# Performance work log

Measured on AMD Instinct MI355X. Metric: run time of the kernel, lower is better.

Reference implementation:

```python
import jax, jax.numpy as jnp
import numpy as np

ALPHA = 0.2          # LeakyReLU negative slope
NEG_BIG = -9e15      # mask fill value from the original code
N, IN_F, OUT_F = 8192, 128, 64


def setup_inputs() -> dict:
    key = jax.random.key(0)
    k1, k2, k3, k4 = jax.random.split(key, 4)
    h = jax.random.normal(k1, (N, IN_F), dtype=jnp.float32)
    adj = jax.random.randint(k2, (N, N), 0, 2, dtype=jnp.int32)
    W = jax.random.normal(k3, (IN_F, OUT_F), dtype=jnp.float32) * 0.1
    a = jax.random.normal(k4, (2 * OUT_F, 1), dtype=jnp.float32) * 0.1
    return {"h": h, "adj": adj, "W": W, "a": a}


def reference(h, adj, W, a):
    # Wh: [N, F]
    Wh = h @ W
    # e_ij = leakyrelu([Wh_i ; Wh_j] . a) = leakyrelu(Wh_i.a1 + Wh_j.a2)
    # (identical math to the original NxNx2F concat, without materializing it)
    a1 = a[:OUT_F, 0]   # [F]
    a2 = a[OUT_F:, 0]   # [F]
    s1 = Wh @ a1        # [N]
    s2 = Wh @ a2        # [N]
    e = jax.nn.leaky_relu(s1[:, None] + s2[None, :], negative_slope=ALPHA)  # [N, N]
    e = jnp.where(adj > 0, e, jnp.float32(NEG_BIG))
    attention = jax.nn.softmax(e, axis=1)
    # dropout is identity at inference (training=False)
    h_prime = attention @ Wh  # [N, F]
    return jax.nn.elu(h_prime)  # concat=True -> elu
```

## Files before the change

### kernel.cpp

```cpp
#include <hip/hip_runtime.h>
#include <hip/hip_bf16.h>

#define N 8192
#define IN_F 128
#define OUT_F 64
#define LRELU_ALPHA 0.2f
#define NEG_BIG -9000000000000000.0f

typedef __attribute__((ext_vector_type(8))) short short8;
typedef __attribute__((ext_vector_type(4))) float float4v;

__device__ __forceinline__ unsigned short bf16_bits(float x) {
  unsigned u = __builtin_bit_cast(unsigned, x);
  u += 0x7fffu + ((u >> 16) & 1u);
  return (unsigned short)(u >> 16);
}

__global__ __launch_bounds__(256) void prep_kernel(
    const float* __restrict__ h, const float* __restrict__ W,
    const float* __restrict__ a, float* __restrict__ s1,
    float* __restrict__ s2, unsigned short* __restrict__ whT) {
  const int tid = threadIdx.x;
  const int row = blockIdx.x * 4 + (tid >> 6);
  const int k = tid & 63;
  const float* hr = h + row * IN_F;
  float acc = 0.f;
#pragma unroll 8
  for (int c = 0; c < IN_F; ++c) acc = fmaf(hr[c], W[c * OUT_F + k], acc);
  whT[(long)k * N + row] = bf16_bits(acc);
  float p1 = acc * a[k];
  float p2 = acc * a[OUT_F + k];
#pragma unroll
  for (int off = 32; off > 0; off >>= 1) {
    p1 += __shfl_xor(p1, off);
    p2 += __shfl_xor(p2, off);
  }
  if (k == 0) { s1[row] = p1; s2[row] = p2; }
}

__global__ __launch_bounds__(512) void gat_kernel(
    const int* __restrict__ adj, const float* __restrict__ s1,
    const float* __restrict__ s2, const unsigned short* __restrict__ whT,
    float* __restrict__ out) {
  __shared__ float lds_acc[8][16][65];
  __shared__ float lds_l[8][16];

  const int tid = threadIdx.x;
  const int wave = tid >> 6;
  const int lane = tid & 63;
  const int r16 = lane & 15;
  const int quad = lane >> 4;
  const int row0 = blockIdx.x * 16;
  const int col0 = wave * 1024;

  const float s1r = s1[row0 + r16];
  const long adj_base = (long)(row0 + r16) * N;

  float lsum = 0.f;
  float4v acc0 = {0.f, 0.f, 0.f, 0.f};
  float4v acc1 = {0.f, 0.f, 0.f, 0.f};
  float4v acc2 = {0.f, 0.f, 0.f, 0.f};
  float4v acc3 = {0.f, 0.f, 0.f, 0.f};

  for (int t = 0; t < 32; ++t) {
    const int j0 = col0 + t * 32 + quad * 8;
    const int4* ap = (const int4*)(adj + adj_base + j0);
    const int4 a0 = ap[0];
    const int4 a1 = ap[1];
    const float4* sp = (const float4*)(s2 + j0);
    const float4 s20 = sp[0], s21 = sp[1];
    const unsigned short* bp = whT + (long)r16 * N + j0;
    const short8 b0 = *(const short8*)(bp + 0L * 16 * N);
    const short8 b1 = *(const short8*)(bp + 1L * 16 * N);
    const short8 b2 = *(const short8*)(bp + 2L * 16 * N);
    const short8 b3 = *(const short8*)(bp + 3L * 16 * N);

    float se[8] = {s20.x, s20.y, s20.z, s20.w, s21.x, s21.y, s21.z, s21.w};
    int am[8] = {a0.x, a0.y, a0.z, a0.w, a1.x, a1.y, a1.z, a1.w};
    short8 afrag;
#pragma unroll
    for (int i = 0; i < 8; ++i) {
      float tv = s1r + se[i];
      tv = fmaxf(tv, LRELU_ALPHA * tv);
      const float e = am[i] > 0 ? tv : NEG_BIG;
      const float p = __expf(e);
      lsum += p;
      afrag[i] = (short)bf16_bits(p);
    }
    acc0 = __builtin_amdgcn_mfma_f32_16x16x32_bf16(afrag, b0, acc0, 0, 0, 0);
    acc1 = __builtin_amdgcn_mfma_f32_16x16x32_bf16(afrag, b1, acc1, 0, 0, 0);
    acc2 = __builtin_amdgcn_mfma_f32_16x16x32_bf16(afrag, b2, acc2, 0, 0, 0);
    acc3 = __builtin_amdgcn_mfma_f32_16x16x32_bf16(afrag, b3, acc3, 0, 0, 0);
  }

  lsum += __shfl_xor(lsum, 16);
  lsum += __shfl_xor(lsum, 32);
  if (lane < 16) lds_l[wave][lane] = lsum;
#pragma unroll
  for (int reg = 0; reg < 4; ++reg) {
    const int r = quad * 4 + reg;
    lds_acc[wave][r][0 * 16 + r16] = acc0[reg];
    lds_acc[wave][r][1 * 16 + r16] = acc1[reg];
    lds_acc[wave][r][2 * 16 + r16] = acc2[reg];
    lds_acc[wave][r][3 * 16 + r16] = acc3[reg];
  }
  __syncthreads();

#pragma unroll
  for (int o = tid; o < 16 * 64; o += 512) {
    const int r = o >> 6, k = o & 63;
    float S = 0.f, L = 0.f;
#pragma unroll
    for (int w = 0; w < 8; ++w) {
      S += lds_acc[w][r][k];
      L += lds_l[w][r];
    }
    const float v = S / L;
    out[(long)(row0 + r) * OUT_F + k] = v > 0.f ? v : expm1f(v);
  }
}

extern "C" void kernel_launch(void* const* d_in, const int* in_sizes, int n_in,
                              void* d_out, int out_size, void* d_ws, size_t ws_size,
                              hipStream_t stream) {
  const float* h = (const float*)d_in[0];
  const int* adj = (const int*)d_in[1];
  const float* W = (const float*)d_in[2];
  const float* a = (const float*)d_in[3];
  float* out = (float*)d_out;

  float* s1 = (float*)d_ws;
  float* s2 = s1 + N;
  unsigned short* whT = (unsigned short*)(s2 + N);

  prep_kernel<<<N / 4, 256, 0, stream>>>(h, W, a, s1, s2, whT);
  gat_kernel<<<N / 16, 512, 0, stream>>>(adj, s1, s2, whT, out);
}
```

Measured before the change: 447.8 us.

## Coalesce adjacency loads via LDS staging and pre-swizzle Wh into MFMA fragment order

The GAT kernel now has each lane read contiguous int4 chunks of adjacency across 16 rows, computes exp weights, and stages the bf16 probabilities in a padded LDS buffer, then reads MFMA A-fragments from LDS. A new repack kernel rearranges Wh into fragment-contiguous order so B-fragment loads are fully coalesced. The row-sum is computed with an extra MFMA against a vector of ones instead of shuffles, and masked entries are set to zero directly rather than exp of a large negative. This adds one extra small kernel launch, LDS traffic and register pressure in exchange for better global load coalescing on the dominant adjacency read.

```diff
diff --git a/kernel.cpp b/kernel.cpp
--- a/kernel.cpp
+++ b/kernel.cpp
@@ -5,10 +5,10 @@
 #define IN_F 128
 #define OUT_F 64
 #define LRELU_ALPHA 0.2f
-#define NEG_BIG -9000000000000000.0f
 
 typedef __attribute__((ext_vector_type(8))) short short8;
 typedef __attribute__((ext_vector_type(4))) float float4v;
+typedef __attribute__((ext_vector_type(4))) unsigned short ushortx4;
 
 __device__ __forceinline__ unsigned short bf16_bits(float x) {
   unsigned u = __builtin_bit_cast(unsigned, x);
@@ -38,84 +38,100 @@
   if (k == 0) { s1[row] = p1; s2[row] = p2; }
 }
 
-__global__ __launch_bounds__(512) void gat_kernel(
+__global__ __launch_bounds__(256) void repack_kernel(
+    const unsigned short* __restrict__ whT, unsigned short* __restrict__ whF) {
+  const int f = blockIdx.x * 256 + threadIdx.x;
+  const int lane = f & 63, tt = (f >> 6) & 3, c = f >> 8;
+  const int r16 = lane & 15, quad = lane >> 4;
+  const short8 v = *(const short8*)(whT + (long)(tt * 16 + r16) * N + c * 32 + quad * 8);
+  *(short8*)(whF + (long)f * 8) = v;
+}
+
+#define PSTR 264
+#define WREG (16 * PSTR * 2)
+
+__global__ __launch_bounds__(512, 4) void gat_kernel(
     const int* __restrict__ adj, const float* __restrict__ s1,
-    const float* __restrict__ s2, const unsigned short* __restrict__ whT,
+    const float* __restrict__ s2, const unsigned short* __restrict__ whF,
     float* __restrict__ out) {
-  __shared__ float lds_acc[8][16][65];
-  __shared__ float lds_l[8][16];
+  __shared__ __align__(16) unsigned char lds_raw[8 * WREG];
+  const int tid = threadIdx.x;
+  const int w = tid >> 6, L = tid & 63;
+  const int r16 = L & 15, quad = L >> 4;
+  const int row0 = blockIdx.x * 16;
+  unsigned short* pl = (unsigned short*)(lds_raw + w * WREG);
 
-  const int tid = threadIdx.x;
-  const int wave = tid >> 6;
-  const int lane = tid & 63;
-  const int r16 = lane & 15;
-  const int quad = lane >> 4;
-  const int row0 = blockIdx.x * 16;
-  const int col0 = wave * 1024;
+  float s1r[16];
+#pragma unroll
+  for (int r = 0; r < 16; ++r) s1r[r] = s1[row0 + r];
 
-  const float s1r = s1[row0 + r16];
-  const long adj_base = (long)(row0 + r16) * N;
-
-  float lsum = 0.f;
   float4v acc0 = {0.f, 0.f, 0.f, 0.f};
   float4v acc1 = {0.f, 0.f, 0.f, 0.f};
   float4v acc2 = {0.f, 0.f, 0.f, 0.f};
   float4v acc3 = {0.f, 0.f, 0.f, 0.f};
+  float4v accL = {0.f, 0.f, 0.f, 0.f};
+  const short ONE = (short)0x3F80;
+  const short8 ones = {ONE, ONE, ONE, ONE, ONE, ONE, ONE, ONE};
 
-  for (int t = 0; t < 32; ++t) {
-    const int j0 = col0 + t * 32 + quad * 8;
-    const int4* ap = (const int4*)(adj + adj_base + j0);
-    const int4 a0 = ap[0];
-    const int4 a1 = ap[1];
-    const float4* sp = (const float4*)(s2 + j0);
-    const float4 s20 = sp[0], s21 = sp[1];
-    const unsigned short* bp = whT + (long)r16 * N + j0;
-    const short8 b0 = *(const short8*)(bp + 0L * 16 * N);
-    const short8 b1 = *(const short8*)(bp + 1L * 16 * N);
-    const short8 b2 = *(const short8*)(bp + 2L * 16 * N);
-    const short8 b3 = *(const short8*)(bp + 3L * 16 * N);
-
-    float se[8] = {s20.x, s20.y, s20.z, s20.w, s21.x, s21.y, s21.z, s21.w};
-    int am[8] = {a0.x, a0.y, a0.z, a0.w, a1.x, a1.y, a1.z, a1.w};
-    short8 afrag;
+  for (int s = 0; s < 4; ++s) {
+    const int col = w * 1024 + s * 256 + L * 4;
+    const float4 s2v = *(const float4*)(s2 + col);
+    int4 av[16];
 #pragma unroll
-    for (int i = 0; i < 8; ++i) {
-      float tv = s1r + se[i];
-      tv = fmaxf(tv, LRELU_ALPHA * tv);
-      const float e = am[i] > 0 ? tv : NEG_BIG;
-      const float p = __expf(e);
-      lsum += p;
-      afrag[i] = (short)bf16_bits(p);
+    for (int r = 0; r < 16; ++r)
+      av[r] = *(const int4*)(adj + (long)(row0 + r) * N + col);
+#pragma unroll
+    for (int r = 0; r < 16; ++r) {
+      float e0 = s1r[r] + s2v.x; e0 = fmaxf(e0, LRELU_ALPHA * e0);
+      float e1 = s1r[r] + s2v.y; e1 = fmaxf(e1, LRELU_ALPHA * e1);
+      float e2 = s1r[r] + s2v.z; e2 = fmaxf(e2, LRELU_ALPHA * e2);
+      float e3 = s1r[r] + s2v.w; e3 = fmaxf(e3, LRELU_ALPHA * e3);
+      const float p0 = av[r].x > 0 ? __expf(e0) : 0.f;
+      const float p1 = av[r].y > 0 ? __expf(e1) : 0.f;
+      const float p2 = av[r].z > 0 ? __expf(e2) : 0.f;
+      const float p3 = av[r].w > 0 ? __expf(e3) : 0.f;
+      ushortx4 pk = {bf16_bits(p0), bf16_bits(p1), bf16_bits(p2), bf16_bits(p3)};
+      *(ushortx4*)(pl + r * PSTR + L * 4) = pk;
     }
-    acc0 = __builtin_amdgcn_mfma_f32_16x16x32_bf16(afrag, b0, acc0, 0, 0, 0);
-    acc1 = __builtin_amdgcn_mfma_f32_16x16x32_bf16(afrag, b1, acc1, 0, 0, 0);
-    acc2 = __builtin_amdgcn_mfma_f32_16x16x32_bf16(afrag, b2, acc2, 0, 0, 0);
-    acc3 = __builtin_amdgcn_mfma_f32_16x16x32_bf16(afrag, b3, acc3, 0, 0, 0);
+#pragma unroll
+    for (int sub = 0; sub < 8; ++sub) {
+      const short8 afrag = *(const short8*)(pl + r16 * PSTR + sub * 32 + quad * 8);
+      const int c32 = w * 32 + s * 8 + sub;
+      const unsigned short* bp = whF + ((long)c32 * 4 * 64 + L) * 8;
+      const short8 b0 = *(const short8*)(bp + 0 * 512);
+      const short8 b1 = *(const short8*)(bp + 1 * 512);
+      const short8 b2 = *(const short8*)(bp + 2 * 512);
+      const short8 b3 = *(const short8*)(bp + 3 * 512);
+      acc0 = __builtin_amdgcn_mfma_f32_16x16x32_bf16(afrag, b0, acc0, 0, 0, 0);
+      acc1 = __builtin_amdgcn_mfma_f32_16x16x32_bf16(afrag, b1, acc1, 0, 0, 0);
+      acc2 = __builtin_amdgcn_mfma_f32_16x16x32_bf16(afrag, b2, acc2, 0, 0, 0);
+      acc3 = __builtin_amdgcn_mfma_f32_16x16x32_bf16(afrag, b3, acc3, 0, 0, 0);
+      accL = __builtin_amdgcn_mfma_f32_16x16x32_bf16(afrag, ones, accL, 0, 0, 0);
+    }
   }
 
-  lsum += __shfl_xor(lsum, 16);
-  lsum += __shfl_xor(lsum, 32);
-  if (lane < 16) lds_l[wave][lane] = lsum;
+  float* F = (float*)pl;
 #pragma unroll
   for (int reg = 0; reg < 4; ++reg) {
     const int r = quad * 4 + reg;
-    lds_acc[wave][r][0 * 16 + r16] = acc0[reg];
-    lds_acc[wave][r][1 * 16 + r16] = acc1[reg];
-    lds_acc[wave][r][2 * 16 + r16] = acc2[reg];
-    lds_acc[wave][r][3 * 16 + r16] = acc3[reg];
+    F[r * 65 + 0 * 16 + r16] = acc0[reg];
+    F[r * 65 + 1 * 16 + r16] = acc1[reg];
+    F[r * 65 + 2 * 16 + r16] = acc2[reg];
+    F[r * 65 + 3 * 16 + r16] = acc3[reg];
+    if (r16 == 0) F[1040 + r] = accL[reg];
   }
   __syncthreads();
 
-#pragma unroll
   for (int o = tid; o < 16 * 64; o += 512) {
     const int r = o >> 6, k = o & 63;
-    float S = 0.f, L = 0.f;
+    float S = 0.f, Lx = 0.f;
 #pragma unroll
-    for (int w = 0; w < 8; ++w) {
-      S += lds_acc[w][r][k];
-      L += lds_l[w][r];
+    for (int ww = 0; ww < 8; ++ww) {
+      const float* Fw = (const float*)(lds_raw + ww * WREG);
+      S += Fw[r * 65 + k];
+      Lx += Fw[1040 + r];
     }
-    const float v = S / L;
+    const float v = S / Lx;
     out[(long)(row0 + r) * OUT_F + k] = v > 0.f ? v : expm1f(v);
   }
 }
@@ -132,7 +148,9 @@
   float* s1 = (float*)d_ws;
   float* s2 = s1 + N;
   unsigned short* whT = (unsigned short*)(s2 + N);
+  unsigned short* whF = whT + (long)OUT_F * N;
 
   prep_kernel<<<N / 4, 256, 0, stream>>>(h, W, a, s1, s2, whT);
-  gat_kernel<<<N / 16, 512, 0, stream>>>(adj, s1, s2, whT, out);
+  repack_kernel<<<N * OUT_F / 8 / 256, 256, 0, stream>>>(whT, whF);
+  gat_kernel<<<N / 16, 512, 0, stream>>>(adj, s1, s2, whF, out);
 }
```

Result: faster. 423.8 us (-5.4%).
